# Optimization experiments

Measured on AMD Instinct MI355X. Metric: run time of the kernel, lower is better.

Reference implementation:

```python
import jax, jax.numpy as jnp
import numpy as np

D_MODEL = 1024
N_HEADS = 16
DEPTH = D_MODEL // N_HEADS
P_FEAT = 64
NEG_BIG = -1.0e9


def setup_inputs() -> dict:
    key = jax.random.key(0)
    ks = jax.random.split(key, 12)
    B, S = 4, 2048
    s = 1.0 / np.sqrt(D_MODEL)
    return {
        "q": jax.random.normal(ks[0], (B, S, D_MODEL), jnp.float32),
        "k": jax.random.normal(ks[1], (B, S, D_MODEL), jnp.float32),
        "v": jax.random.normal(ks[2], (B, S, D_MODEL), jnp.float32),
        "protocol_features": jax.random.normal(ks[3], (B, P_FEAT), jnp.float32),
        "mask": jax.random.randint(ks[4], (B, 1, 1, S), 0, 2).astype(jnp.float32),
        "wq": jax.random.normal(ks[5], (D_MODEL, D_MODEL), jnp.float32) * s,
        "bq": jnp.zeros((D_MODEL,), jnp.float32),
        "wk": jax.random.normal(ks[6], (D_MODEL, D_MODEL), jnp.float32) * s,
        "bk": jnp.zeros((D_MODEL,), jnp.float32),
        "wv": jax.random.normal(ks[7], (D_MODEL, D_MODEL), jnp.float32) * s,
        "bv": jnp.zeros((D_MODEL,), jnp.float32),
        "wg": jax.random.normal(ks[8], (P_FEAT, N_HEADS), jnp.float32) * (1.0 / np.sqrt(P_FEAT)),
        "bg": jnp.zeros((N_HEADS,), jnp.float32),
    }


def _split_heads(x, B):
    # [B,S,d_model] -> [B,H,S,depth]
    return x.reshape(B, -1, N_HEADS, DEPTH).transpose(0, 2, 1, 3)


def reference(q, k, v, protocol_features, mask, wq, bq, wk, bk, wv, bv, wg, bg):
    B = q.shape[0]
    qh = _split_heads(q @ wq + bq, B)
    kh = _split_heads(k @ wk + bk, B)
    vh = _split_heads(v @ wv + bv, B)
    # scaled QK^T: [B,H,S,S]
    logits = jnp.einsum("bhqd,bhkd->bhqk", qh, kh) / jnp.sqrt(jnp.float32(DEPTH))
    # per-head protocol gate (sigmoid), broadcast over q/k positions
    validity = jax.nn.sigmoid(protocol_features @ wg + bg)  # [B,H]
    logits = logits * validity[:, :, None, None]
    logits = logits + mask * NEG_BIG
    attn = jax.nn.softmax(logits, axis=-1)
    out = jnp.einsum("bhqk,bhkd->bhqd", attn, vh)
    concat = out.transpose(0, 2, 1, 3).reshape(B, -1, D_MODEL)
    return concat, attn
```

## Files before the change

kernel.cpp:

```cpp
#include <hip/hip_runtime.h>

#define S_LEN 2048
#define NB 4
#define NH 16
#define BHN 64
#define DM 1024
#define DEP 64
#define MROWS 8192

typedef __attribute__((ext_vector_type(8))) short short8;
typedef __attribute__((ext_vector_type(4))) float f32x4;

#define MFMA_BF16(a, b, c) __builtin_amdgcn_mfma_f32_16x16x32_bf16((a), (b), (c), 0, 0, 0)

typedef __attribute__((address_space(1))) const void* as1cv;
typedef __attribute__((address_space(3))) void* as3v;

__device__ __forceinline__ void gld16(const void* g, void* l) {
  __builtin_amdgcn_global_load_lds((as1cv)g, (as3v)l, 16, 0, 0);
}

__device__ __forceinline__ unsigned short f2bf(float f) {
  unsigned u = __float_as_uint(f);
  u += 0x7fffu + ((u >> 16) & 1u);
  return (unsigned short)(u >> 16);
}

__device__ __forceinline__ unsigned cvtpk(float a, float b) {
  unsigned r;
  asm("v_cvt_pk_bf16_f32 %0, %1, %2" : "=v"(r) : "v"(a), "v"(b));
  return r;
}

__device__ __forceinline__ int SWZ(int row, int gran) {
  return row * 64 + ((gran ^ (row & 7)) << 3);
}

__global__ void gate_kernel(const float* __restrict__ pf, const float* __restrict__ wg,
                            const float* __restrict__ bg, float* __restrict__ validity) {
  int t = threadIdx.x;
  int b = t >> 4, h = t & 15;
  float s = bg[h];
  for (int i = 0; i < 64; i++) s += pf[b * 64 + i] * wg[i * NH + h];
  validity[t] = 1.0f / (1.0f + __expf(-s));
}

__global__ __launch_bounds__(256) void wt_kernel(const float* __restrict__ W,
                                                 unsigned short* __restrict__ Wt) {
  __shared__ unsigned short T[64][72];
  int k0 = blockIdx.x * 64, n0 = blockIdx.y * 64;
  int t = threadIdx.x;
  int r = t >> 2, c4 = (t & 3) * 16;
  for (int j = 0; j < 16; j += 4) {
    float4 v = *(const float4*)&W[(size_t)(k0 + r) * DM + n0 + c4 + j];
    T[r][c4 + j + 0] = f2bf(v.x); T[r][c4 + j + 1] = f2bf(v.y);
    T[r][c4 + j + 2] = f2bf(v.z); T[r][c4 + j + 3] = f2bf(v.w);
  }
  __syncthreads();
  union { unsigned short us[16]; uint4 v[2]; } o;
  for (int j = 0; j < 16; j++) o.us[j] = T[c4 + j][r];
  *(uint4*)&Wt[(size_t)(n0 + r) * DM + k0 + c4] = o.v[0];
  *(uint4*)&Wt[(size_t)(n0 + r) * DM + k0 + c4 + 8] = o.v[1];
}

__global__ __launch_bounds__(256) void vt_kernel(const unsigned short* __restrict__ vh,
                                                 unsigned short* __restrict__ vhT) {
  __shared__ unsigned short T[64][72];
  int bh = blockIdx.y;
  int s0 = blockIdx.x * 64;
  int t = threadIdx.x;
  int r = t >> 2, c4 = (t & 3) * 16;
  const unsigned short* src = vh + ((size_t)bh * S_LEN + s0 + r) * DEP + c4;
  *(uint4*)&T[r][c4] = *(const uint4*)src;
  *(uint4*)&T[r][c4 + 8] = *(const uint4*)(src + 8);
  __syncthreads();
  union { unsigned short us[16]; uint4 v[2]; } o;
  for (int j = 0; j < 16; j++) o.us[j] = T[c4 + j][r];
  unsigned short* dst = vhT + ((size_t)bh * DEP + r) * S_LEN + s0 + c4;
  *(uint4*)dst = o.v[0];
  *(uint4*)(dst + 8) = o.v[1];
}

__global__ __launch_bounds__(256) void proj3_gemm(const float* __restrict__ Xq,
                                                  const float* __restrict__ Xk,
                                                  const float* __restrict__ Xv,
                                                  const unsigned short* __restrict__ BtBase,
                                                  const float* __restrict__ bq,
                                                  const float* __restrict__ bk,
                                                  const float* __restrict__ bv,
                                                  unsigned short* __restrict__ Ybase) {
  __shared__ unsigned short As[128 * 64], Bs[128 * 64];
  const int K = DM;
  int z = blockIdx.z;
  const float* X = (z == 0) ? Xq : (z == 1) ? Xk : Xv;
  const float* bias = (z == 0) ? bq : (z == 1) ? bk : bv;
  const unsigned short* Bt = BtBase + (size_t)z * DM * DM;
  unsigned short* Y = Ybase + (size_t)z * MROWS * DM;

  int tid = threadIdx.x, w = tid >> 6, l = tid & 63, g = l >> 4, lc = l & 15;
  int r0 = blockIdx.x * 128, c0 = blockIdx.y * 128;
  int wr = w >> 1, wc = w & 1;
  int lrow = l >> 3, lcol = (l & 7) * 8;
  int sr = tid >> 3, sc = (tid & 7) * 8;
  f32x4 acc[4][4] = {};
  for (int k0 = 0; k0 < K; k0 += 64) {
    __syncthreads();
    for (int i = 0; i < 4; i++) {
      int row = (w * 4 + i) * 8 + lrow;
      gld16(Bt + (size_t)(c0 + row) * K + k0 + lcol, &Bs[(w * 4 + i) * 512]);
    }
    for (int i = 0; i < 4; i++) {
      int row = i * 32 + sr;
      const float* src = X + (size_t)(r0 + row) * K + k0 + sc;
      float4 a0 = *(const float4*)src;
      float4 a1 = *(const float4*)(src + 4);
      uint4 o = {cvtpk(a0.x, a0.y), cvtpk(a0.z, a0.w),
                 cvtpk(a1.x, a1.y), cvtpk(a1.z, a1.w)};
      *(uint4*)&As[row * 64 + sc] = o;
    }
    __syncthreads();
    for (int kk = 0; kk < 2; kk++) {
      short8 a[4], b[4];
      for (int m = 0; m < 4; m++)
        a[m] = *(const short8*)&As[(wr * 64 + m * 16 + lc) * 64 + kk * 32 + g * 8];
      for (int n = 0; n < 4; n++)
        b[n] = *(const short8*)&Bs[(wc * 64 + n * 16 + lc) * 64 + kk * 32 + g * 8];
      for (int m = 0; m < 4; m++)
        for (int n = 0; n < 4; n++)
          acc[m][n] = MFMA_BF16(a[m], b[n], acc[m][n]);
    }
  }
  for (int n = 0; n < 4; n++) {
    int c = c0 + wc * 64 + n * 16 + lc;
    float bi = bias[c];
    int h = c >> 6, d = c & 63;
    for (int m = 0; m < 4; m++) {
      int rowbase = r0 + wr * 64 + m * 16 + g * 4;
      for (int r = 0; r < 4; r++) {
        int row = rowbase + r;
        int b_ = row >> 11, s = row & 2047;
        Y[(((size_t)b_ * NH + h) * S_LEN + s) * DEP + d] = f2bf(acc[m][n][r] + bi);
      }
    }
  }
}

__global__ __launch_bounds__(512) void attn_fused(const unsigned short* __restrict__ qh,
                                                  const unsigned short* __restrict__ kh,
                                                  const unsigned short* __restrict__ vhT,
                                                  const float* __restrict__ validity,
                                                  const float* __restrict__ mask,
                                                  float* __restrict__ concat,
                                                  float* __restrict__ attn) {
  __shared__ union {
    unsigned short Q[128 * 64];
    float PF[8][16 * 68];
  } QP;
  __shared__ unsigned short KV[4][64 * 64];
  __shared__ float Ms[S_LEN];

  int id = blockIdx.x;
  int cxcd = id & 7, j = id >> 3;
  int bh = cxcd * 8 + (j >> 4);
  int q0 = (j & 15) * 128;
  int b = bh >> 4, h = bh & 15;

  int tid = threadIdx.x, w = tid >> 6, l = tid & 63, g = l >> 4, lc = l & 15;
  int srow = l >> 3;
  int sgran = (l & 7) ^ srow;
  float scale = validity[bh] * 0.125f * 1.44269504f;
  for (int i = tid; i < S_LEN; i += 512)
    Ms[i] = mask[(size_t)b * S_LEN + i] * (-1.44269504e9f);

  const unsigned short* qb = qh + (size_t)bh * S_LEN * DEP;
  const unsigned short* kb = kh + (size_t)bh * S_LEN * DEP;
  const unsigned short* vb = vhT + (size_t)bh * DEP * S_LEN;
  int qrow = w * 16 + lc;

  unsigned short* B0 = &KV[0][0];
  unsigned short* B1 = &KV[2][0];
  for (int i = 0; i < 2; i++)
    gld16(qb + (size_t)(q0 + i * 64 + w * 8 + srow) * DEP + sgran * 8,
          &QP.Q[(i * 64 + w * 8) * 64]);
  for (int i = 0; i < 2; i++)
    gld16(kb + (size_t)(i * 64 + w * 8 + srow) * DEP + sgran * 8,
          B0 + (i * 64 + w * 8) * 64);
  __syncthreads();
  short8 aq0 = *(const short8*)&QP.Q[SWZ(qrow, g)];
  short8 aq1 = *(const short8*)&QP.Q[SWZ(qrow, 4 + g)];

  float ell[4] = {0.f, 0.f, 0.f, 0.f};
  for (int kt2 = 0; kt2 < 16; kt2++) {
    const int cb = kt2 & 1;
    unsigned short* cur = cb ? B1 : B0;
    if (kt2 < 15) {
      unsigned short* nxt = cb ? B0 : B1;
      for (int i = 0; i < 2; i++)
        gld16(kb + (size_t)((kt2 + 1) * 128 + i * 64 + w * 8 + srow) * DEP + sgran * 8,
              nxt + (i * 64 + w * 8) * 64);
    }
    __builtin_amdgcn_sched_barrier(0);
    if (kt2 < 15) { asm volatile("s_waitcnt vmcnt(2)" ::: "memory"); }
    else          { asm volatile("s_waitcnt vmcnt(0)" ::: "memory"); }
    __builtin_amdgcn_sched_barrier(0);
    for (int f = 0; f < 8; f++) {
      int krow = f * 16 + lc;
      short8 b0 = *(const short8*)&cur[SWZ(krow, g)];
      short8 b1 = *(const short8*)&cur[SWZ(krow, 4 + g)];
      f32x4 c = {};
      __builtin_amdgcn_s_setprio(1);
      c = MFMA_BF16(aq0, b0, c);
      c = MFMA_BF16(aq1, b1, c);
      __builtin_amdgcn_s_setprio(0);
      float mb = Ms[kt2 * 128 + f * 16 + lc];
      for (int r = 0; r < 4; r++) ell[r] += exp2f(fmaf(c[r], scale, mb));
    }
    __builtin_amdgcn_s_barrier();
  }
  for (int m = 8; m >= 1; m >>= 1)
    for (int r = 0; r < 4; r++) ell[r] += __shfl_xor(ell[r], m, 64);
  float rinv[4];
  for (int r = 0; r < 4; r++) rinv[r] = 1.0f / ell[r];

  gld16(kb + (size_t)(w * 8 + srow) * DEP + sgran * 8, &KV[0][w * 512]);
  gld16(vb + (size_t)(w * 8 + srow) * S_LEN + sgran * 8, &KV[2][w * 512]);
  __syncthreads();

  float* PFw = QP.PF[w];
  float* arow2 = attn + ((size_t)bh * S_LEN + q0 + w * 16 + lc) * S_LEN + g * 8;

  f32x4 O[4] = {};
#pragma unroll 2
  for (int kt = 0; kt < 32; kt++) {
    const int cb = kt & 1;
    if (kt < 31) {
      gld16(kb + (size_t)((kt + 1) * 64 + w * 8 + srow) * DEP + sgran * 8,
            &KV[cb ^ 1][w * 512]);
      gld16(vb + (size_t)(w * 8 + srow) * S_LEN + (kt + 1) * 64 + sgran * 8,
            &KV[2 + (cb ^ 1)][w * 512]);
    }
    __builtin_amdgcn_sched_barrier(0);
    if (kt < 31) { asm volatile("s_waitcnt vmcnt(6)" ::: "memory"); }
    else         { asm volatile("s_waitcnt vmcnt(4)" ::: "memory"); }
    __builtin_amdgcn_sched_barrier(0);
    for (int f = 0; f < 4; f++) {
      int krow = f * 16 + lc;
      short8 b0 = *(const short8*)&KV[cb][SWZ(krow, g)];
      short8 b1 = *(const short8*)&KV[cb][SWZ(krow, 4 + g)];
      f32x4 c = {};
      __builtin_amdgcn_s_setprio(1);
      c = MFMA_BF16(aq0, b0, c);
      c = MFMA_BF16(aq1, b1, c);
      __builtin_amdgcn_s_setprio(0);
      float mb = Ms[kt * 64 + f * 16 + lc];
      for (int r = 0; r < 4; r++) {
        float p = exp2f(fmaf(c[r], scale, mb)) * rinv[r];
        PFw[(g * 4 + r) * 68 + f * 16 + lc] = p;
      }
    }
    f32x4 t0 = *(const f32x4*)&PFw[lc * 68 + g * 8];
    f32x4 t1 = *(const f32x4*)&PFw[lc * 68 + g * 8 + 4];
    f32x4 t2 = *(const f32x4*)&PFw[lc * 68 + 32 + g * 8];
    f32x4 t3 = *(const f32x4*)&PFw[lc * 68 + 32 + g * 8 + 4];
    union { uint4 u; short8 s; } pk0, pk1;
    pk0.u = uint4{cvtpk(t0[0], t0[1]), cvtpk(t0[2], t0[3]),
                  cvtpk(t1[0], t1[1]), cvtpk(t1[2], t1[3])};
    pk1.u = uint4{cvtpk(t2[0], t2[1]), cvtpk(t2[2], t2[3]),
                  cvtpk(t3[0], t3[1]), cvtpk(t3[2], t3[3])};
    *(f32x4*)(arow2 + kt * 64) = t0;
    *(f32x4*)(arow2 + kt * 64 + 4) = t1;
    *(f32x4*)(arow2 + kt * 64 + 32) = t2;
    *(f32x4*)(arow2 + kt * 64 + 36) = t3;
    __builtin_amdgcn_s_setprio(1);
    for (int n = 0; n < 4; n++) {
      int vrow = n * 16 + lc;
      short8 v0 = *(const short8*)&KV[2 + cb][SWZ(vrow, g)];
      short8 v1 = *(const short8*)&KV[2 + cb][SWZ(vrow, 4 + g)];
      O[n] = MFMA_BF16(pk0.s, v0, O[n]);
      O[n] = MFMA_BF16(pk1.s, v1, O[n]);
    }
    __builtin_amdgcn_s_setprio(0);
    __builtin_amdgcn_s_barrier();
  }
  for (int n = 0; n < 4; n++)
    for (int r = 0; r < 4; r++)
      concat[((size_t)b * S_LEN + q0 + w * 16 + g * 4 + r) * DM + h * DEP + n * 16 + lc] =
          O[n][r];
}

extern "C" void kernel_launch(void* const* d_in, const int* in_sizes, int n_in,
                              void* d_out, int out_size, void* d_ws, size_t ws_size,
                              hipStream_t stream) {
  const float* q    = (const float*)d_in[0];
  const float* k    = (const float*)d_in[1];
  const float* v    = (const float*)d_in[2];
  const float* pf   = (const float*)d_in[3];
  const float* mask = (const float*)d_in[4];
  const float* wq   = (const float*)d_in[5];
  const float* bq   = (const float*)d_in[6];
  const float* wk   = (const float*)d_in[7];
  const float* bk   = (const float*)d_in[8];
  const float* wv   = (const float*)d_in[9];
  const float* bv   = (const float*)d_in[10];
  const float* wg   = (const float*)d_in[11];
  const float* bg   = (const float*)d_in[12];

  float* concat = (float*)d_out;
  float* attn   = concat + (size_t)NB * S_LEN * DM;

  unsigned short* wqT = (unsigned short*)attn;
  unsigned short* wkT = wqT + (size_t)DM * DM;
  unsigned short* wvT = wkT + (size_t)DM * DM;

  float* validity = (float*)d_ws;
  unsigned short* qhp = (unsigned short*)((char*)d_ws + 4096);
  unsigned short* khp = qhp + (size_t)MROWS * DM;
  unsigned short* vhp = khp + (size_t)MROWS * DM;
  unsigned short* vhT = vhp + (size_t)MROWS * DM;

  gate_kernel<<<1, 64, 0, stream>>>(pf, wg, bg, validity);

  wt_kernel<<<dim3(16, 16), 256, 0, stream>>>(wq, wqT);
  wt_kernel<<<dim3(16, 16), 256, 0, stream>>>(wk, wkT);
  wt_kernel<<<dim3(16, 16), 256, 0, stream>>>(wv, wvT);

  proj3_gemm<<<dim3(64, 8, 3), 256, 0, stream>>>(q, k, v, wqT, bq, bk, bv, qhp);

  vt_kernel<<<dim3(32, 64), 256, 0, stream>>>(vhp, vhT);

  attn_fused<<<1024, 512, 0, stream>>>(qhp, khp, vhT, validity, mask, concat, attn);
}
```

Baseline: 480.0 us.

## Transpose QK MFMA operands to keep P in registers for PV

Swaps the K and Q operands of the score MFMA so each lane holds four consecutive key columns of P. Those values can then feed a 16x16x16 bf16 MFMA for the PV product directly from registers, with no fp32 LDS staging buffer and transpose. Mask bias is stored in LDS as bf16, and the row-sum reduction shrinks to a single scalar per lane. The vmcnt waits now sit at the end of each iteration to cover the next buffer. The trade-off is twice as many smaller PV MFMAs and a changed wait and store-count discipline.

```diff
diff --git a/kernel.cpp b/kernel.cpp
--- a/kernel.cpp
+++ b/kernel.cpp
@@ -9,9 +9,14 @@
 #define MROWS 8192
 
 typedef __attribute__((ext_vector_type(8))) short short8;
+typedef __attribute__((ext_vector_type(4))) short s16x4;
 typedef __attribute__((ext_vector_type(4))) float f32x4;
 
 #define MFMA_BF16(a, b, c) __builtin_amdgcn_mfma_f32_16x16x32_bf16((a), (b), (c), 0, 0, 0)
+
+__device__ __forceinline__ void mfma16(const s16x4& a, const s16x4& b, f32x4& c) {
+  asm("v_mfma_f32_16x16x16_bf16 %0, %1, %2, %0" : "+v"(c) : "v"(a), "v"(b));
+}
 
 typedef __attribute__((address_space(1))) const void* as1cv;
 typedef __attribute__((address_space(3))) void* as3v;
@@ -152,12 +157,9 @@
                                                   const float* __restrict__ mask,
                                                   float* __restrict__ concat,
                                                   float* __restrict__ attn) {
-  __shared__ union {
-    unsigned short Q[128 * 64];
-    float PF[8][16 * 68];
-  } QP;
+  __shared__ unsigned short Qs[128 * 64];
   __shared__ unsigned short KV[4][64 * 64];
-  __shared__ float Ms[S_LEN];
+  __shared__ unsigned short MsB[S_LEN];
 
   int id = blockIdx.x;
   int cxcd = id & 7, j = id >> 3;
@@ -170,7 +172,7 @@
   int sgran = (l & 7) ^ srow;
   float scale = validity[bh] * 0.125f * 1.44269504f;
   for (int i = tid; i < S_LEN; i += 512)
-    Ms[i] = mask[(size_t)b * S_LEN + i] * (-1.44269504e9f);
+    MsB[i] = f2bf(mask[(size_t)b * S_LEN + i] * (-1.44269504e9f));
 
   const unsigned short* qb = qh + (size_t)bh * S_LEN * DEP;
   const unsigned short* kb = kh + (size_t)bh * S_LEN * DEP;
@@ -181,15 +183,15 @@
   unsigned short* B1 = &KV[2][0];
   for (int i = 0; i < 2; i++)
     gld16(qb + (size_t)(q0 + i * 64 + w * 8 + srow) * DEP + sgran * 8,
-          &QP.Q[(i * 64 + w * 8) * 64]);
+          &Qs[(i * 64 + w * 8) * 64]);
   for (int i = 0; i < 2; i++)
     gld16(kb + (size_t)(i * 64 + w * 8 + srow) * DEP + sgran * 8,
           B0 + (i * 64 + w * 8) * 64);
   __syncthreads();
-  short8 aq0 = *(const short8*)&QP.Q[SWZ(qrow, g)];
-  short8 aq1 = *(const short8*)&QP.Q[SWZ(qrow, 4 + g)];
-
-  float ell[4] = {0.f, 0.f, 0.f, 0.f};
+  short8 aq0 = *(const short8*)&Qs[SWZ(qrow, g)];
+  short8 aq1 = *(const short8*)&Qs[SWZ(qrow, 4 + g)];
+
+  float ell = 0.f;
   for (int kt2 = 0; kt2 < 16; kt2++) {
     const int cb = kt2 & 1;
     unsigned short* cur = cb ? B1 : B0;
@@ -199,35 +201,37 @@
         gld16(kb + (size_t)((kt2 + 1) * 128 + i * 64 + w * 8 + srow) * DEP + sgran * 8,
               nxt + (i * 64 + w * 8) * 64);
     }
-    __builtin_amdgcn_sched_barrier(0);
-    if (kt2 < 15) { asm volatile("s_waitcnt vmcnt(2)" ::: "memory"); }
-    else          { asm volatile("s_waitcnt vmcnt(0)" ::: "memory"); }
-    __builtin_amdgcn_sched_barrier(0);
     for (int f = 0; f < 8; f++) {
       int krow = f * 16 + lc;
-      short8 b0 = *(const short8*)&cur[SWZ(krow, g)];
-      short8 b1 = *(const short8*)&cur[SWZ(krow, 4 + g)];
+      short8 ak0 = *(const short8*)&cur[SWZ(krow, g)];
+      short8 ak1 = *(const short8*)&cur[SWZ(krow, 4 + g)];
       f32x4 c = {};
       __builtin_amdgcn_s_setprio(1);
-      c = MFMA_BF16(aq0, b0, c);
-      c = MFMA_BF16(aq1, b1, c);
+      c = MFMA_BF16(ak0, aq0, c);
+      c = MFMA_BF16(ak1, aq1, c);
       __builtin_amdgcn_s_setprio(0);
-      float mb = Ms[kt2 * 128 + f * 16 + lc];
-      for (int r = 0; r < 4; r++) ell[r] += exp2f(fmaf(c[r], scale, mb));
-    }
+      uint2 mu = *(const uint2*)&MsB[kt2 * 128 + f * 16 + g * 4];
+      float mb0 = __uint_as_float(mu.x << 16);
+      float mb1 = __uint_as_float(mu.x & 0xFFFF0000u);
+      float mb2 = __uint_as_float(mu.y << 16);
+      float mb3 = __uint_as_float(mu.y & 0xFFFF0000u);
+      ell += exp2f(fmaf(c[0], scale, mb0)) + exp2f(fmaf(c[1], scale, mb1)) +
+             exp2f(fmaf(c[2], scale, mb2)) + exp2f(fmaf(c[3], scale, mb3));
+    }
+    __builtin_amdgcn_sched_barrier(0);
+    asm volatile("s_waitcnt vmcnt(0)" ::: "memory");
+    __builtin_amdgcn_sched_barrier(0);
     __builtin_amdgcn_s_barrier();
   }
-  for (int m = 8; m >= 1; m >>= 1)
-    for (int r = 0; r < 4; r++) ell[r] += __shfl_xor(ell[r], m, 64);
-  float rinv[4];
-  for (int r = 0; r < 4; r++) rinv[r] = 1.0f / ell[r];
+  ell += __shfl_xor(ell, 16, 64);
+  ell += __shfl_xor(ell, 32, 64);
+  float rinv = 1.0f / ell;
 
   gld16(kb + (size_t)(w * 8 + srow) * DEP + sgran * 8, &KV[0][w * 512]);
   gld16(vb + (size_t)(w * 8 + srow) * S_LEN + sgran * 8, &KV[2][w * 512]);
   __syncthreads();
 
-  float* PFw = QP.PF[w];
-  float* arow2 = attn + ((size_t)bh * S_LEN + q0 + w * 16 + lc) * S_LEN + g * 8;
+  float* arow = attn + ((size_t)bh * S_LEN + q0 + w * 16 + lc) * S_LEN + g * 4;
 
   f32x4 O[4] = {};
 #pragma unroll 2
@@ -239,47 +243,47 @@
       gld16(vb + (size_t)(w * 8 + srow) * S_LEN + (kt + 1) * 64 + sgran * 8,
             &KV[2 + (cb ^ 1)][w * 512]);
     }
-    __builtin_amdgcn_sched_barrier(0);
-    if (kt < 31) { asm volatile("s_waitcnt vmcnt(6)" ::: "memory"); }
-    else         { asm volatile("s_waitcnt vmcnt(4)" ::: "memory"); }
-    __builtin_amdgcn_sched_barrier(0);
+    s16x4 pa[4];
+#pragma unroll
     for (int f = 0; f < 4; f++) {
       int krow = f * 16 + lc;
-      short8 b0 = *(const short8*)&KV[cb][SWZ(krow, g)];
-      short8 b1 = *(const short8*)&KV[cb][SWZ(krow, 4 + g)];
+      short8 ak0 = *(const short8*)&KV[cb][SWZ(krow, g)];
+      short8 ak1 = *(const short8*)&KV[cb][SWZ(krow, 4 + g)];
       f32x4 c = {};
       __builtin_amdgcn_s_setprio(1);
-      c = MFMA_BF16(aq0, b0, c);
-      c = MFMA_BF16(aq1, b1, c);
+      c = MFMA_BF16(ak0, aq0, c);
+      c = MFMA_BF16(ak1, aq1, c);
       __builtin_amdgcn_s_setprio(0);
-      float mb = Ms[kt * 64 + f * 16 + lc];
-      for (int r = 0; r < 4; r++) {
-        float p = exp2f(fmaf(c[r], scale, mb)) * rinv[r];
-        PFw[(g * 4 + r) * 68 + f * 16 + lc] = p;
+      uint2 mu = *(const uint2*)&MsB[kt * 64 + f * 16 + g * 4];
+      float mb0 = __uint_as_float(mu.x << 16);
+      float mb1 = __uint_as_float(mu.x & 0xFFFF0000u);
+      float mb2 = __uint_as_float(mu.y << 16);
+      float mb3 = __uint_as_float(mu.y & 0xFFFF0000u);
+      float p0 = exp2f(fmaf(c[0], scale, mb0)) * rinv;
+      float p1 = exp2f(fmaf(c[1], scale, mb1)) * rinv;
+      float p2 = exp2f(fmaf(c[2], scale, mb2)) * rinv;
+      float p3 = exp2f(fmaf(c[3], scale, mb3)) * rinv;
+      *(f32x4*)(arow + kt * 64 + f * 16) = f32x4{p0, p1, p2, p3};
+      union { unsigned u[2]; s16x4 s; } pk;
+      pk.u[0] = cvtpk(p0, p1);
+      pk.u[1] = cvtpk(p2, p3);
+      pa[f] = pk.s;
+    }
+    __builtin_amdgcn_s_setprio(1);
+#pragma unroll
+    for (int f = 0; f < 4; f++) {
+#pragma unroll
+      for (int n = 0; n < 4; n++) {
+        int vrow = n * 16 + lc;
+        int gran = (f * 2 + (g >> 1)) ^ (vrow & 7);
+        s16x4 bv = *(const s16x4*)&KV[2 + cb][vrow * 64 + gran * 8 + (g & 1) * 4];
+        mfma16(pa[f], bv, O[n]);
       }
     }
-    f32x4 t0 = *(const f32x4*)&PFw[lc * 68 + g * 8];
-    f32x4 t1 = *(const f32x4*)&PFw[lc * 68 + g * 8 + 4];
-    f32x4 t2 = *(const f32x4*)&PFw[lc * 68 + 32 + g * 8];
-    f32x4 t3 = *(const f32x4*)&PFw[lc * 68 + 32 + g * 8 + 4];
-    union { uint4 u; short8 s; } pk0, pk1;
-    pk0.u = uint4{cvtpk(t0[0], t0[1]), cvtpk(t0[2], t0[3]),
-                  cvtpk(t1[0], t1[1]), cvtpk(t1[2], t1[3])};
-    pk1.u = uint4{cvtpk(t2[0], t2[1]), cvtpk(t2[2], t2[3]),
-                  cvtpk(t3[0], t3[1]), cvtpk(t3[2], t3[3])};
-    *(f32x4*)(arow2 + kt * 64) = t0;
-    *(f32x4*)(arow2 + kt * 64 + 4) = t1;
-    *(f32x4*)(arow2 + kt * 64 + 32) = t2;
-    *(f32x4*)(arow2 + kt * 64 + 36) = t3;
-    __builtin_amdgcn_s_setprio(1);
-    for (int n = 0; n < 4; n++) {
-      int vrow = n * 16 + lc;
-      short8 v0 = *(const short8*)&KV[2 + cb][SWZ(vrow, g)];
-      short8 v1 = *(const short8*)&KV[2 + cb][SWZ(vrow, 4 + g)];
-      O[n] = MFMA_BF16(pk0.s, v0, O[n]);
-      O[n] = MFMA_BF16(pk1.s, v1, O[n]);
-    }
     __builtin_amdgcn_s_setprio(0);
+    __builtin_amdgcn_sched_barrier(0);
+    if (kt < 31) { asm volatile("s_waitcnt vmcnt(4)" ::: "memory"); }
+    __builtin_amdgcn_sched_barrier(0);
     __builtin_amdgcn_s_barrier();
   }
   for (int n = 0; n < 4; n++)
```

New measurement: 456.6 us. 4.9% less time.
